# Kernel tuning notes

Hardware: AMD Instinct MI355X
Metric: run time of the kernel (lower is better)

Reference implementation:

```python
import jax, jax.numpy as jnp
import numpy as np

NEG_INF = -100000000.0  # matches masked_fill value in torch source

def setup_inputs() -> dict:
    key = jax.random.key(0)
    ks = jax.random.split(key, 7)
    d_model, d = 1024, 128
    B, S = 4, 2048
    scale = 1.0 / np.sqrt(d_model)
    x = jax.random.normal(ks[0], (B, S, d_model), dtype=jnp.float32)
    Wq = jax.random.normal(ks[1], (d, d_model), dtype=jnp.float32) * scale
    bq = jax.random.normal(ks[2], (d,), dtype=jnp.float32) * 0.02
    Wk = jax.random.normal(ks[3], (d, d_model), dtype=jnp.float32) * scale
    bk = jax.random.normal(ks[4], (d,), dtype=jnp.float32) * 0.02
    Wv = jax.random.normal(ks[5], (d, d_model), dtype=jnp.float32) * scale
    bv = jax.random.normal(ks[6], (d,), dtype=jnp.float32) * 0.02
    return {"x": x, "Wq": Wq, "bq": bq, "Wk": Wk, "bk": bk, "Wv": Wv, "bv": bv}

def reference(x, Wq, bq, Wk, bk, Wv, bv):
    # Q,K,V: [B,S,d] via torch Linear (x @ W.T + b)
    Q = jnp.einsum('bsm,dm->bsd', x, Wq) + bq
    K = jnp.einsum('bsm,dm->bsd', x, Wk) + bk
    V = jnp.einsum('bsm,dm->bsd', x, Wv) + bv
    d = Wk.shape[0]
    scale = 1.0 / jnp.sqrt(jnp.asarray(d, dtype=Q.dtype))
    scores = jnp.einsum('bqd,bkd->bqk', Q, K) * scale  # [B,S,S]
    # Faithful to source: tril then value-based mask (tril==0 -> -1e8).
    tril = jnp.tril(scores)
    masked = jnp.where(tril == 0, NEG_INF, tril)
    attn = jax.nn.softmax(masked, axis=-1)
    context = jnp.einsum('bqk,bkd->bqd', attn, V)
    return context
```

## Files before the change

kernel.cpp:

```cpp
#include <hip/hip_runtime.h>

typedef __attribute__((ext_vector_type(8))) short bf16x8;
typedef __attribute__((ext_vector_type(4))) float f32x4;

__device__ __forceinline__ unsigned short f2bf(float f) {
    unsigned int u = __float_as_uint(f);
    u += 0x7fffu + ((u >> 16) & 1u);
    return (unsigned short)(u >> 16);
}
__device__ __forceinline__ float bf2f(unsigned short h) {
    return __uint_as_float((unsigned int)h << 16);
}
__device__ __forceinline__ unsigned int pack2bf(float lo, float hi) {
    return (unsigned int)f2bf(lo) | ((unsigned int)f2bf(hi) << 16);
}
__device__ __forceinline__ void async_ld16(void* lds, const void* g) {
    __builtin_amdgcn_global_load_lds(
        (const __attribute__((address_space(1))) unsigned int*)g,
        (__attribute__((address_space(3))) unsigned int*)lds, 16, 0, 0);
}

__global__ __launch_bounds__(256) void conv_w(
    const float* __restrict__ Wq, const float* __restrict__ Wk,
    const float* __restrict__ Wv, const float* __restrict__ x,
    unsigned short* __restrict__ Wcat, unsigned short* __restrict__ xb)
{
    int j = blockIdx.x * 256 + threadIdx.x;
    const float* src;
    unsigned short* dst;
    if (j < 49152) {
        size_t o = (size_t)j * 8;
        int sel = (int)(o >> 17);
        const float* W = (sel == 0) ? Wq : ((sel == 1) ? Wk : Wv);
        src = W + (o & 131071);
        dst = Wcat + o;
    } else {
        size_t o = (size_t)(j - 49152) * 8;
        src = x + o;
        dst = xb + o;
    }
    float4 f0 = ((const float4*)src)[0];
    float4 f1 = ((const float4*)src)[1];
    uint4 u;
    u.x = pack2bf(f0.x, f0.y); u.y = pack2bf(f0.z, f0.w);
    u.z = pack2bf(f1.x, f1.y); u.w = pack2bf(f1.z, f1.w);
    *(uint4*)dst = u;
}

__global__ __launch_bounds__(256) void qkv_gemm(
    const unsigned short* __restrict__ xb,
    const unsigned short* __restrict__ Wcat,
    const float* __restrict__ bq, const float* __restrict__ bk,
    const float* __restrict__ bv,
    unsigned short* __restrict__ Qf,
    unsigned short* __restrict__ Kf,
    unsigned short* __restrict__ Vf)
{
    __shared__ unsigned short As[2][32 * 64];
    __shared__ unsigned short Bs[2][128 * 64];

    const int tid  = threadIdx.x;
    const int lane = tid & 63;
    const int w    = tid >> 6;
    const int quad = lane >> 4;
    const int ln   = lane & 15;
    const int lr   = lane >> 3;
    const int csw  = ((lane & 7) ^ lr) * 8;

    const int bid   = blockIdx.x;
    const int nb    = bid >> 8;
    const int mbase = (bid & 255) * 32;
    const unsigned short* Wsel = Wcat + (size_t)nb * 128 * 1024;

    const int arow = tid >> 3;
    const int acol = ((tid & 7) ^ (arow & 7)) * 8;
    const unsigned short* asrc = xb + (size_t)(mbase + arow) * 1024 + acol;

    f32x4 acc[2][2];
#pragma unroll
    for (int mt = 0; mt < 2; mt++)
#pragma unroll
        for (int nt = 0; nt < 2; nt++) acc[mt][nt] = (f32x4){0.f, 0.f, 0.f, 0.f};

    auto stageB = [&](int kb, int p) {
        const int kcol = kb * 64 + csw;
#pragma unroll
        for (int j = 0; j < 4; j++) {
            int chunk = w * 4 + j;
            async_ld16(&Bs[p][chunk * 512 + lane * 8],
                       Wsel + (size_t)(chunk * 8 + lr) * 1024 + kcol);
        }
    };
    auto stageA = [&](int kb, int p) {
        async_ld16(&As[p][tid * 8], asrc + kb * 64);
    };

    stageB(0, 0);
    stageA(0, 0);
    __syncthreads();

    for (int kb = 0; kb < 16; kb++) {
        const int p = kb & 1;
        if (kb < 15) {
            stageB(kb + 1, p ^ 1);
            stageA(kb + 1, p ^ 1);
        }
#pragma unroll
        for (int ks = 0; ks < 2; ks++) {
            bf16x8 a[2], b[2];
#pragma unroll
            for (int mt = 0; mt < 2; mt++) {
                int row = mt * 16 + ln;
                a[mt] = *(const bf16x8*)&As[p][row * 64 + ((ks * 4 + quad) ^ (ln & 7)) * 8];
            }
#pragma unroll
            for (int nt = 0; nt < 2; nt++) {
                int row = w * 32 + nt * 16 + ln;
                b[nt] = *(const bf16x8*)&Bs[p][row * 64 + ((ks * 4 + quad) ^ (ln & 7)) * 8];
            }
#pragma unroll
            for (int mt = 0; mt < 2; mt++)
#pragma unroll
                for (int nt = 0; nt < 2; nt++)
                    acc[mt][nt] = __builtin_amdgcn_mfma_f32_16x16x32_bf16(
                        a[mt], b[nt], acc[mt][nt], 0, 0, 0);
        }
        __syncthreads();
    }

    const float scale = (nb == 0) ? 0.08838834764831845f : 1.0f;
    const float* bsel = (nb == 0) ? bq : ((nb == 1) ? bk : bv);
    float bias_v[2];
#pragma unroll
    for (int nt = 0; nt < 2; nt++) bias_v[nt] = bsel[w * 32 + nt * 16 + ln];

    if (nb == 0) {
#pragma unroll
        for (int mt = 0; mt < 2; mt++)
#pragma unroll
            for (int nt = 0; nt < 2; nt++)
#pragma unroll
                for (int r = 0; r < 4; r++) {
                    int m = mbase + mt * 16 + quad * 4 + r;
                    int d = w * 32 + nt * 16 + ln;
                    int bb = m >> 11, s = m & 2047;
                    int qq = s >> 6, j = s & 63, wv = j >> 4, lnq = j & 15;
                    int ksd = d >> 5, rr = d & 31, qd = rr >> 3, e = rr & 7;
                    size_t idx = (((size_t)((bb * 32 + qq) * 4 + wv) * 4 + ksd) * 64
                                  + qd * 16 + lnq) * 8 + e;
                    Qf[idx] = f2bf((acc[mt][nt][r] + bias_v[nt]) * scale);
                }
    } else if (nb == 1) {
#pragma unroll
        for (int mt = 0; mt < 2; mt++)
#pragma unroll
            for (int nt = 0; nt < 2; nt++)
#pragma unroll
                for (int r = 0; r < 4; r++) {
                    int m = mbase + mt * 16 + quad * 4 + r;
                    int d = w * 32 + nt * 16 + ln;
                    int bb = m >> 11, s = m & 2047;
                    int kt = s >> 6, j = s & 63, ct = j >> 4, lnk = j & 15;
                    int ksd = d >> 5, rr = d & 31, qd = rr >> 3, e = rr & 7;
                    size_t idx = (((size_t)(bb * 128 + kt * 4 + ct) * 4 + ksd) * 64
                                  + qd * 16 + lnk) * 8 + e;
                    Kf[idx] = f2bf(acc[mt][nt][r] + bias_v[nt]);
                }
    } else {
#pragma unroll
        for (int mt = 0; mt < 2; mt++)
#pragma unroll
            for (int nt = 0; nt < 2; nt++) {
                int dd = w * 32 + nt * 16 + ln;
                int m0 = mbase + mt * 16 + quad * 4;
                int bb = m0 >> 11, s0 = m0 & 2047;
                int kt = s0 >> 6, j0 = s0 & 63;
                int kstep = j0 >> 5, rr0 = j0 & 31, qdv = rr0 >> 3, e0 = rr0 & 7;
                int dt = dd >> 4, lnv = dd & 15;
                size_t base = ((((size_t)(bb * 32 + kt) * 2 + kstep) * 8 + dt) * 64
                               + qdv * 16 + lnv) * 8 + e0;
                ushort4 u = { f2bf(acc[mt][nt][0] + bias_v[nt]),
                              f2bf(acc[mt][nt][1] + bias_v[nt]),
                              f2bf(acc[mt][nt][2] + bias_v[nt]),
                              f2bf(acc[mt][nt][3] + bias_v[nt]) };
                *(ushort4*)&Vf[base] = u;
            }
    }
}

__global__ __launch_bounds__(256) void flash_attn(
    const unsigned short* __restrict__ Qf,
    const unsigned short* __restrict__ Kf,
    const unsigned short* __restrict__ Vf,
    unsigned short* __restrict__ Opart,
    float* __restrict__ lsum_g,
    float* __restrict__ out)
{
    __shared__ unsigned short Pl[64][72];

    int j = blockIdx.x;
    const int b = j / 144;
    int t = j % 144;
    int q = 0, c = 0;
#pragma unroll 1
    for (int qq = 0; qq < 32; qq++) {
        int ncq = (qq >> 2) + 1;
        if (t < ncq) { q = qq; c = t; break; }
        t -= ncq;
    }
    const int m4 = q >> 2, r4 = q & 3;
    const int nc = m4 + 1;
    const int pbase = b * 144 + q + 2 * m4 * (m4 - 1) + r4 * m4;
    const int pidx  = pbase + c;
    const int k0 = c * 4;
    const int kend = (c * 4 + 4 < q + 1) ? (c * 4 + 4) : (q + 1);

    const int tid  = threadIdx.x;
    const int lane = tid & 63, w = tid >> 6, quad = lane >> 4, ln = lane & 15;
    const float M0 = 16.0f;

    bf16x8 qa[4];
    const unsigned short* qbt =
        Qf + (size_t)((b * 32 + q) * 4 + w) * 2048 + lane * 8;
#pragma unroll
    for (int ks = 0; ks < 4; ks++)
        qa[ks] = *(const bf16x8*)(qbt + (size_t)ks * 512);

    float l_i[4];
    f32x4 Ofr[8];
#pragma unroll
    for (int r = 0; r < 4; r++) l_i[r] = 0.f;
#pragma unroll
    for (int dt = 0; dt < 8; dt++) Ofr[dt] = (f32x4){0.f, 0.f, 0.f, 0.f};

    for (int kt = k0; kt < kend; kt++) {
        const unsigned short* kbt = Kf + (size_t)(b * 128 + kt * 4) * 2048 + lane * 8;
        const unsigned short* vbt = Vf + (size_t)(b * 32 + kt) * 8192 + lane * 8;
        bf16x8 kf[4][4], vf[2][8];
#pragma unroll
        for (int ct = 0; ct < 4; ct++)
#pragma unroll
            for (int ks = 0; ks < 4; ks++)
                kf[ct][ks] = *(const bf16x8*)(kbt + (size_t)(ct * 4 + ks) * 512);
#pragma unroll
        for (int kstep = 0; kstep < 2; kstep++)
#pragma unroll
            for (int dt = 0; dt < 8; dt++)
                vf[kstep][dt] = *(const bf16x8*)(vbt + (size_t)(kstep * 8 + dt) * 512);

        f32x4 sfr[4];
#pragma unroll
        for (int ct = 0; ct < 4; ct++) {
            f32x4 s = (f32x4){0.f, 0.f, 0.f, 0.f};
#pragma unroll
            for (int ks = 0; ks < 4; ks++)
                s = __builtin_amdgcn_mfma_f32_16x16x32_bf16(qa[ks], kf[ct][ks], s, 0, 0, 0);
            sfr[ct] = s;
        }

        if (kt == q) {
#pragma unroll
            for (int ct = 0; ct < 4; ct++)
#pragma unroll
                for (int r = 0; r < 4; r++)
                    if (ct * 16 + ln > w * 16 + quad * 4 + r)
                        sfr[ct][r] = -__builtin_inff();
        }

#pragma unroll
        for (int ct = 0; ct < 4; ct++)
#pragma unroll
            for (int r = 0; r < 4; r++) {
                float pv = __expf(sfr[ct][r] - M0);
                l_i[r] += pv;
                Pl[w * 16 + quad * 4 + r][ct * 16 + ln] = f2bf(pv);
            }

#pragma unroll
        for (int kstep = 0; kstep < 2; kstep++) {
            bf16x8 pa = *(const bf16x8*)&Pl[w * 16 + ln][kstep * 32 + quad * 8];
#pragma unroll
            for (int dt = 0; dt < 8; dt++)
                Ofr[dt] = __builtin_amdgcn_mfma_f32_16x16x32_bf16(pa, vf[kstep][dt], Ofr[dt], 0, 0, 0);
        }
    }

#pragma unroll
    for (int off = 1; off < 16; off <<= 1)
#pragma unroll
        for (int r = 0; r < 4; r++) l_i[r] += __shfl_xor(l_i[r], off, 64);

    if (nc == 1) {
        float inv_[4];
#pragma unroll
        for (int r = 0; r < 4; r++) inv_[r] = 1.0f / l_i[r];
#pragma unroll
        for (int dt = 0; dt < 8; dt++)
#pragma unroll
            for (int r = 0; r < 4; r++) {
                int row = w * 16 + quad * 4 + r;
                out[((size_t)(b * 2048 + q * 64 + row)) * 128 + dt * 16 + ln] =
                    Ofr[dt][r] * inv_[r];
            }
        return;
    }

#pragma unroll
    for (int dt = 0; dt < 8; dt++) {
        ushort4 u = { f2bf(Ofr[dt][0]), f2bf(Ofr[dt][1]),
                      f2bf(Ofr[dt][2]), f2bf(Ofr[dt][3]) };
        *(ushort4*)&Opart[(((size_t)pidx * 8 + dt) * 4 + w) * 256 + lane * 4] = u;
    }
    if (ln == 0) {
#pragma unroll
        for (int r = 0; r < 4; r++)
            lsum_g[(size_t)pidx * 64 + w * 16 + quad * 4 + r] = l_i[r];
    }
}

__global__ __launch_bounds__(256) void combine(
    const unsigned short* __restrict__ Opart,
    const float* __restrict__ lsum_g,
    float* __restrict__ out)
{
    const int j = blockIdx.x;
    const int b = j / 28;
    const int q = (j % 28) + 4;
    const int m4 = q >> 2, r4 = q & 3;
    const int nc = m4 + 1;
    const int pbase = b * 144 + q + 2 * m4 * (m4 - 1) + r4 * m4;

    const int tid  = threadIdx.x;
    const int lane = tid & 63, w = tid >> 6, quad = lane >> 4, ln = lane & 15;

    float lt[4] = {0.f, 0.f, 0.f, 0.f};
    f32x4 Ofr[8];
#pragma unroll
    for (int dt = 0; dt < 8; dt++) Ofr[dt] = (f32x4){0.f, 0.f, 0.f, 0.f};

#pragma unroll 1
    for (int c2 = 0; c2 < nc; c2++) {
        const size_t pb2 = (size_t)(pbase + c2);
#pragma unroll
        for (int r = 0; r < 4; r++)
            lt[r] += lsum_g[pb2 * 64 + w * 16 + quad * 4 + r];
#pragma unroll
        for (int dt = 0; dt < 8; dt++) {
            ushort4 u = *(const ushort4*)&Opart[((pb2 * 8 + dt) * 4 + w) * 256 + lane * 4];
            Ofr[dt][0] += bf2f(u.x);
            Ofr[dt][1] += bf2f(u.y);
            Ofr[dt][2] += bf2f(u.z);
            Ofr[dt][3] += bf2f(u.w);
        }
    }
    float inv_[4];
#pragma unroll
    for (int r = 0; r < 4; r++) inv_[r] = 1.0f / lt[r];
#pragma unroll
    for (int dt = 0; dt < 8; dt++)
#pragma unroll
        for (int r = 0; r < 4; r++) {
            int row = w * 16 + quad * 4 + r;
            out[((size_t)(b * 2048 + q * 64 + row)) * 128 + dt * 16 + ln] =
                Ofr[dt][r] * inv_[r];
        }
}

extern "C" void kernel_launch(void* const* d_in, const int* in_sizes, int n_in,
                              void* d_out, int out_size, void* d_ws, size_t ws_size,
                              hipStream_t stream) {
    const float* x  = (const float*)d_in[0];
    const float* Wq = (const float*)d_in[1];
    const float* bq = (const float*)d_in[2];
    const float* Wk = (const float*)d_in[3];
    const float* bk = (const float*)d_in[4];
    const float* Wv = (const float*)d_in[5];
    const float* bv = (const float*)d_in[6];
    float* out = (float*)d_out;

    char* wsb = (char*)d_ws;
    unsigned short* Opart = (unsigned short*)wsb;
    float*          lsum  = (float*)(wsb + 9437184);
    unsigned short* Wcat  = (unsigned short*)(wsb + 10485760);
    unsigned short* Qf    = (unsigned short*)(wsb + 11272192);
    unsigned short* Kf    = Qf + (size_t)8192 * 128;
    unsigned short* Vf    = Qf + (size_t)2 * 8192 * 128;
    unsigned short* xb    = (unsigned short*)(wsb + 17563648);

    conv_w<<<4288, 256, 0, stream>>>(Wq, Wk, Wv, x, Wcat, xb);
    qkv_gemm<<<768, 256, 0, stream>>>(xb, Wcat, bq, bk, bv, Qf, Kf, Vf);
    flash_attn<<<576, 256, 0, stream>>>(Qf, Kf, Vf, Opart, lsum, out);
    combine<<<112, 256, 0, stream>>>(Opart, lsum, out);
}
```

Before: 126.4 us.

## Fuse x bf16 conversion into QKV GEMM and split attention into single-wave blocks

Drops the separate fp32-to-bf16 conversion of x. The QKV GEMM now loads fp32 x tiles straight into LDS with a swizzle and converts to bf16 using v_cvt_pk_bf16_f32 when forming MFMA operands, which removes one full write and read of the bf16 copy of x. The flash attention kernel is relaunched as one 64-thread wave per block, four times as many blocks, with a smaller LDS buffer, for finer scheduling granularity. The trade-off is doubled LDS traffic for A in the GEMM, extra conversion instructions, and some redundant block-index decoding in the attention kernel.

```diff
diff --git a/kernel.cpp b/kernel.cpp
--- a/kernel.cpp
+++ b/kernel.cpp
@@ -14,6 +14,11 @@
 __device__ __forceinline__ unsigned int pack2bf(float lo, float hi) {
     return (unsigned int)f2bf(lo) | ((unsigned int)f2bf(hi) << 16);
 }
+__device__ __forceinline__ unsigned int cvtpk(float a, float b) {
+    unsigned int r;
+    asm("v_cvt_pk_bf16_f32 %0, %1, %2" : "=v"(r) : "v"(a), "v"(b));
+    return r;
+}
 __device__ __forceinline__ void async_ld16(void* lds, const void* g) {
     __builtin_amdgcn_global_load_lds(
         (const __attribute__((address_space(1))) unsigned int*)g,
@@ -22,33 +27,22 @@
 
 __global__ __launch_bounds__(256) void conv_w(
     const float* __restrict__ Wq, const float* __restrict__ Wk,
-    const float* __restrict__ Wv, const float* __restrict__ x,
-    unsigned short* __restrict__ Wcat, unsigned short* __restrict__ xb)
+    const float* __restrict__ Wv, unsigned short* __restrict__ Wcat)
 {
-    int j = blockIdx.x * 256 + threadIdx.x;
-    const float* src;
-    unsigned short* dst;
-    if (j < 49152) {
-        size_t o = (size_t)j * 8;
-        int sel = (int)(o >> 17);
-        const float* W = (sel == 0) ? Wq : ((sel == 1) ? Wk : Wv);
-        src = W + (o & 131071);
-        dst = Wcat + o;
-    } else {
-        size_t o = (size_t)(j - 49152) * 8;
-        src = x + o;
-        dst = xb + o;
-    }
+    size_t o = ((size_t)blockIdx.x * 256 + threadIdx.x) * 8;
+    int sel = (int)(o >> 17);
+    const float* W = (sel == 0) ? Wq : ((sel == 1) ? Wk : Wv);
+    const float* src = W + (o & 131071);
     float4 f0 = ((const float4*)src)[0];
     float4 f1 = ((const float4*)src)[1];
     uint4 u;
     u.x = pack2bf(f0.x, f0.y); u.y = pack2bf(f0.z, f0.w);
     u.z = pack2bf(f1.x, f1.y); u.w = pack2bf(f1.z, f1.w);
-    *(uint4*)dst = u;
-}
-
-__global__ __launch_bounds__(256) void qkv_gemm(
-    const unsigned short* __restrict__ xb,
+    *(uint4*)(Wcat + o) = u;
+}
+
+__global__ __launch_bounds__(256, 3) void qkv_gemm(
+    const float* __restrict__ x,
     const unsigned short* __restrict__ Wcat,
     const float* __restrict__ bq, const float* __restrict__ bk,
     const float* __restrict__ bv,
@@ -56,7 +50,7 @@
     unsigned short* __restrict__ Kf,
     unsigned short* __restrict__ Vf)
 {
-    __shared__ unsigned short As[2][32 * 64];
+    __shared__ float Asf[2][32 * 64];
     __shared__ unsigned short Bs[2][128 * 64];
 
     const int tid  = threadIdx.x;
@@ -72,9 +66,11 @@
     const int mbase = (bid & 255) * 32;
     const unsigned short* Wsel = Wcat + (size_t)nb * 128 * 1024;
 
-    const int arow = tid >> 3;
-    const int acol = ((tid & 7) ^ (arow & 7)) * 8;
-    const unsigned short* asrc = xb + (size_t)(mbase + arow) * 1024 + acol;
+    const int g0 = tid, g1 = tid + 256;
+    const float* asrc0 = x + (size_t)(mbase + (g0 >> 4)) * 1024
+                           + (size_t)(((g0 & 15) ^ ((g0 >> 4) & 15)) * 4);
+    const float* asrc1 = x + (size_t)(mbase + (g1 >> 4)) * 1024
+                           + (size_t)(((g1 & 15) ^ ((g1 >> 4) & 15)) * 4);
 
     f32x4 acc[2][2];
 #pragma unroll
@@ -92,7 +88,17 @@
         }
     };
     auto stageA = [&](int kb, int p) {
-        async_ld16(&As[p][tid * 8], asrc + kb * 64);
+        async_ld16(&Asf[p][g0 * 4], asrc0 + kb * 64);
+        async_ld16(&Asf[p][g1 * 4], asrc1 + kb * 64);
+    };
+    auto readA = [&](int p, int mt, int ks) -> bf16x8 {
+        const int r = mt * 16 + ln;
+        const int J = ks * 4 + quad;
+        float4 lo = *(const float4*)&Asf[p][r * 64 + (((2 * J)    ) ^ (r & 15)) * 4];
+        float4 hi = *(const float4*)&Asf[p][r * 64 + (((2 * J + 1)) ^ (r & 15)) * 4];
+        uint4 u = { cvtpk(lo.x, lo.y), cvtpk(lo.z, lo.w),
+                    cvtpk(hi.x, hi.y), cvtpk(hi.z, hi.w) };
+        return *reinterpret_cast<const bf16x8*>(&u);
     };
 
     stageB(0, 0);
@@ -109,10 +115,7 @@
         for (int ks = 0; ks < 2; ks++) {
             bf16x8 a[2], b[2];
 #pragma unroll
-            for (int mt = 0; mt < 2; mt++) {
-                int row = mt * 16 + ln;
-                a[mt] = *(const bf16x8*)&As[p][row * 64 + ((ks * 4 + quad) ^ (ln & 7)) * 8];
-            }
+            for (int mt = 0; mt < 2; mt++) a[mt] = readA(p, mt, ks);
 #pragma unroll
             for (int nt = 0; nt < 2; nt++) {
                 int row = w * 32 + nt * 16 + ln;
@@ -188,7 +191,7 @@
     }
 }
 
-__global__ __launch_bounds__(256) void flash_attn(
+__global__ __launch_bounds__(64, 2) void flash_attn(
     const unsigned short* __restrict__ Qf,
     const unsigned short* __restrict__ Kf,
     const unsigned short* __restrict__ Vf,
@@ -196,9 +199,10 @@
     float* __restrict__ lsum_g,
     float* __restrict__ out)
 {
-    __shared__ unsigned short Pl[64][72];
-
-    int j = blockIdx.x;
+    __shared__ unsigned short Pl[16][72];
+
+    const int w = blockIdx.x & 3;
+    int j = blockIdx.x >> 2;
     const int b = j / 144;
     int t = j % 144;
     int q = 0, c = 0;
@@ -215,8 +219,7 @@
     const int k0 = c * 4;
     const int kend = (c * 4 + 4 < q + 1) ? (c * 4 + 4) : (q + 1);
 
-    const int tid  = threadIdx.x;
-    const int lane = tid & 63, w = tid >> 6, quad = lane >> 4, ln = lane & 15;
+    const int lane = threadIdx.x & 63, quad = lane >> 4, ln = lane & 15;
     const float M0 = 16.0f;
 
     bf16x8 qa[4];
@@ -273,12 +276,12 @@
             for (int r = 0; r < 4; r++) {
                 float pv = __expf(sfr[ct][r] - M0);
                 l_i[r] += pv;
-                Pl[w * 16 + quad * 4 + r][ct * 16 + ln] = f2bf(pv);
+                Pl[quad * 4 + r][ct * 16 + ln] = f2bf(pv);
             }
 
 #pragma unroll
         for (int kstep = 0; kstep < 2; kstep++) {
-            bf16x8 pa = *(const bf16x8*)&Pl[w * 16 + ln][kstep * 32 + quad * 8];
+            bf16x8 pa = *(const bf16x8*)&Pl[ln][kstep * 32 + quad * 8];
 #pragma unroll
             for (int dt = 0; dt < 8; dt++)
                 Ofr[dt] = __builtin_amdgcn_mfma_f32_16x16x32_bf16(pa, vf[kstep][dt], Ofr[dt], 0, 0, 0);
@@ -385,10 +388,9 @@
     unsigned short* Qf    = (unsigned short*)(wsb + 11272192);
     unsigned short* Kf    = Qf + (size_t)8192 * 128;
     unsigned short* Vf    = Qf + (size_t)2 * 8192 * 128;
-    unsigned short* xb    = (unsigned short*)(wsb + 17563648);
-
-    conv_w<<<4288, 256, 0, stream>>>(Wq, Wk, Wv, x, Wcat, xb);
-    qkv_gemm<<<768, 256, 0, stream>>>(xb, Wcat, bq, bk, bv, Qf, Kf, Vf);
-    flash_attn<<<576, 256, 0, stream>>>(Qf, Kf, Vf, Opart, lsum, out);
+
+    conv_w<<<192, 256, 0, stream>>>(Wq, Wk, Wv, Wcat);
+    qkv_gemm<<<768, 256, 0, stream>>>(x, Wcat, bq, bk, bv, Qf, Kf, Vf);
+    flash_attn<<<2304, 64, 0, stream>>>(Qf, Kf, Vf, Opart, lsum, out);
     combine<<<112, 256, 0, stream>>>(Opart, lsum, out);
 }
```

New measurement: 118.8 us. 6.0% less time.
